# Kernel tuning notes

Measured on AMD Instinct MI355X. Metric: run time of the kernel, lower is better.

## Reference

```python
import jax, jax.numpy as jnp
import numpy as np

B, D_IN, H1, H2, A = 8192, 512, 4096, 4096, 64
QMIN, QMAX = -128.0, 127.0  # int8 saturation range


def _int_vals(key, shape, spread):
    # integer-valued fixed-point tensor stored as float32
    return jnp.clip(jnp.round(jax.random.normal(key, shape) * spread), QMIN * spread, QMAX * spread).astype(jnp.float32)


def setup_inputs() -> dict:
    key = jax.random.key(0)
    ks = jax.random.split(key, 9)
    x = jnp.clip(jnp.round(jax.random.normal(ks[0], (B, D_IN)) * 32.0), QMIN, QMAX).astype(jnp.float32)
    w1 = jnp.clip(jnp.round(jax.random.normal(ks[1], (H1, D_IN)) * 16.0), QMIN, QMAX).astype(jnp.float32)
    b1 = _int_vals(ks[2], (H1,), 256.0)
    w2 = jnp.clip(jnp.round(jax.random.normal(ks[3], (H2, H1)) * 16.0), QMIN, QMAX).astype(jnp.float32)
    b2 = _int_vals(ks[4], (H2,), 256.0)
    w_mu = jnp.clip(jnp.round(jax.random.normal(ks[5], (A, H2)) * 16.0), QMIN, QMAX).astype(jnp.float32)
    b_mu = _int_vals(ks[6], (A,), 256.0)
    w_prob = jnp.clip(jnp.round(jax.random.normal(ks[7], (A, H2)) * 16.0), QMIN, QMAX).astype(jnp.float32)
    b_prob = _int_vals(ks[8], (A,), 256.0)
    M = jnp.full((1,), 2.0 ** -10, dtype=jnp.float32)  # per-layer requant multiplier
    s = jnp.full((1,), 0.05, dtype=jnp.float32)        # activation quantize scale
    return {
        "x": x, "w1": w1, "b1": b1, "w2": w2, "b2": b2,
        "w_mu": w_mu, "b_mu": b_mu, "w_prob": w_prob, "b_prob": b_prob,
        "M1": M, "M2": M, "M_mu": M, "M_prob": M,
        "s2": s, "s_mu": s, "s_prob": s,
    }


def _qlinear(x, w, b, M):
    # genesys fixed-point linear: int accumulate then requantize by multiplier M
    acc = jnp.matmul(x, w.T) + b  # integer-valued fp32 accumulator
    return jnp.round(M * acc)


def _quantize(src, scale, zero_point=0.0):
    return jnp.clip(jnp.round(src / scale) + zero_point, QMIN, QMAX)


def reference(x, w1, b1, w2, b2, w_mu, b_mu, w_prob, b_prob, M1, M2, M_mu, M_prob, s2, s_mu, s_prob):
    h = jax.nn.relu(_qlinear(x, w1, b1, M1))
    h = _quantize(h, s2)
    h = jax.nn.relu(_qlinear(h, w2, b2, M2))
    # NOTE: original forward_int feeds the un-quantized relu output into the
    # heads (x_mu/x_prob quantizations are dead code) and returns only prob.
    prob = _qlinear(h, w_prob, b_prob, M_prob)
    return prob
```

## Files before the change

### kernel.cpp

```cpp
#include <hip/hip_runtime.h>
#include <stdint.h>

#define NB   8192
#define DIN  512
#define NH1  4096
#define NH2  4096
#define NA   64

typedef int v4i __attribute__((ext_vector_type(4)));

__device__ __forceinline__ v4i mfma_i8(v4i a, v4i b, v4i c) {
    return __builtin_amdgcn_mfma_i32_16x16x64_i8(a, b, c, 0, 0, 0);
}

__device__ __forceinline__ void gload16(const void* g, const void* l) {
    __builtin_amdgcn_global_load_lds(
        (const __attribute__((address_space(1))) void*)(uintptr_t)g,
        (__attribute__((address_space(3))) void*)(uint32_t)(uintptr_t)l,
        16, 0, 0);
}

__global__ void cvt_i8(const float* __restrict__ in, signed char* __restrict__ out, int n4) {
    const int i = blockIdx.x * blockDim.x + threadIdx.x;
    if (i >= n4) return;
    const float4 v = ((const float4*)in)[i];
    char4 c;
    c.x = (signed char)__float2int_rn(v.x);
    c.y = (signed char)__float2int_rn(v.y);
    c.z = (signed char)__float2int_rn(v.z);
    c.w = (signed char)__float2int_rn(v.w);
    ((char4*)out)[i] = c;
}

__global__ void sum_wp(const float* __restrict__ wp, int* __restrict__ S) {
    __shared__ int red[256];
    const int a = blockIdx.x, t = threadIdx.x;
    int p = 0;
    for (int k = t; k < NH2; k += 256) p += __float2int_rn(wp[(size_t)a * NH2 + k]);
    red[t] = p; __syncthreads();
    for (int s = 128; s > 0; s >>= 1) { if (t < s) red[t] += red[t + s]; __syncthreads(); }
    if (t == 0) S[a] = red[0];
}

template <int EPI>
__global__ __launch_bounds__(256, 2)
void gemm_pl(const signed char* __restrict__ Ag,
             const signed char* __restrict__ Bg,
             int M, int N, int K,
             const float* __restrict__ bias,
             const float* __restrict__ Mscale,
             const float* __restrict__ qscale,
             signed char* __restrict__ out0,
             signed char* __restrict__ out1)
{
    __shared__ __align__(16) signed char lds[3][24576];

    const int tid  = threadIdx.x;
    const int lane = tid & 63;
    const int wid  = tid >> 6;
    const int wm   = wid >> 1, wn = wid & 1;

    const int nwg  = gridDim.x;
    const int bid  = blockIdx.x;
    const int swzb = (bid & 7) * (nwg >> 3) + (bid >> 3);
    const int nbx  = N >> 7;
    const int bx   = swzb % nbx;
    const int by   = swzb / nbx;
    const int bm0  = by << 8, bn0 = bx << 7;

    const int srow = tid >> 2;
    const int sc   = (((tid & 3) ^ ((tid >> 3) & 3)) << 4);
    const signed char* aS = Ag + (size_t)(bm0 + srow) * K + sc;
    const signed char* bS = Bg + (size_t)(bn0 + srow) * K + sc;
    const size_t sK = (size_t)64 * K;

#define STG(bp, t) do { \
    const int ko_ = (t) << 6; \
    gload16(aS + ko_,          &lds[bp][0]     + tid * 16); \
    gload16(aS + sK + ko_,     &lds[bp][4096]  + tid * 16); \
    gload16(aS + 2 * sK + ko_, &lds[bp][8192]  + tid * 16); \
    gload16(aS + 3 * sK + ko_, &lds[bp][12288] + tid * 16); \
    gload16(bS + ko_,          &lds[bp][16384] + tid * 16); \
    gload16(bS + sK + ko_,     &lds[bp][20480] + tid * 16); } while (0)

    const int r    = lane & 15;
    const int pc   = (((lane >> 4) ^ ((r >> 1) & 3)) << 4);
    const int aoff = wm * 8192 + r * 64 + pc;
    const int boff = 16384 + wn * 4096 + r * 64 + pc;

    const int nt = K >> 6;

    STG(0, 0);
    STG(1, 1);
    asm volatile("s_waitcnt vmcnt(6)" ::: "memory");
    __builtin_amdgcn_s_barrier();

    v4i af[8], bf[4];
    {
        const signed char* L = &lds[0][0];
        #pragma unroll
        for (int m = 0; m < 8; ++m) af[m] = *(const v4i*)(L + aoff + m * 1024);
        #pragma unroll
        for (int n = 0; n < 4; ++n) bf[n] = *(const v4i*)(L + boff + n * 1024);
    }

    v4i acc[8][4] = {};
    int cur = 0;

    for (int t = 0; t < nt; ++t) {
        if (t + 2 < nt) {
            const int nb = (cur == 0) ? 2 : cur - 1;
            STG(nb, t + 2);
            asm volatile("s_waitcnt vmcnt(6)" ::: "memory");
        } else {
            asm volatile("s_waitcnt vmcnt(0)" ::: "memory");
        }
        __builtin_amdgcn_s_barrier();

        const int nxt = (cur == 2) ? 0 : cur + 1;
        const signed char* Ln = &lds[nxt][0];

        __builtin_amdgcn_s_setprio(1);
        #pragma unroll
        for (int m = 0; m < 8; ++m) {
            #pragma unroll
            for (int n = 0; n < 4; ++n)
                acc[m][n] = mfma_i8(af[m], bf[n], acc[m][n]);
            af[m] = *(const v4i*)(Ln + aoff + m * 1024);
        }
        __builtin_amdgcn_s_setprio(0);
        #pragma unroll
        for (int n = 0; n < 4; ++n) bf[n] = *(const v4i*)(Ln + boff + n * 1024);

        __builtin_amdgcn_s_barrier();
        cur = nxt;
    }
#undef STG

    __syncthreads();
    signed char* img0 = (signed char*)&lds[0][0];
    signed char* img1 = img0 + 36864;
    const int fr = (lane >> 4) << 2;
    const int fc = lane & 15;

#define FLUSH(dst, img) do { \
    _Pragma("unroll") \
    for (int p = 0; p < 8; ++p) { \
        const int idx = p * 256 + tid; \
        const int row = idx >> 3, ch = (idx & 7) << 4; \
        *(int4*)((dst) + (size_t)(bm0 + row) * N + bn0 + ch) = *(const int4*)((img) + row * 144 + ch); \
    } } while (0)

    if constexpr (EPI == 1) {
        const float Mv = Mscale[0];
        const float sv = qscale[0];
        #pragma unroll
        for (int n = 0; n < 4; ++n) {
            const int ecol = wn * 64 + n * 16 + fc;
            const int bint = __float2int_rn(bias[bn0 + ecol]);
            #pragma unroll
            for (int m = 0; m < 8; ++m) {
                const int erow = wm * 128 + m * 16 + fr;
                #pragma unroll
                for (int j = 0; j < 4; ++j) {
                    const int accv = acc[m][n][j] + bint;
                    float h = rintf(Mv * (float)accv);
                    h = fmaxf(h, 0.0f);
                    float q = rintf(h / sv);
                    q = fminf(fmaxf(q, -128.0f), 127.0f);
                    img0[(erow + j) * 144 + ecol] = (signed char)(int)q;
                }
            }
        }
        __syncthreads();
        FLUSH(out0, img0);
    } else {
        const float Mv = Mscale[0];
        #pragma unroll
        for (int n = 0; n < 4; ++n) {
            const int ecol = wn * 64 + n * 16 + fc;
            const int bint = __float2int_rn(bias[bn0 + ecol]);
            #pragma unroll
            for (int m = 0; m < 8; ++m) {
                const int erow = wm * 128 + m * 16 + fr;
                #pragma unroll
                for (int j = 0; j < 4; ++j) {
                    const int accv = acc[m][n][j] + bint;
                    double rr = rint((double)Mv * (double)accv);
                    rr = rr > 0.0 ? rr : 0.0;
                    const int v = (int)rr;
                    img0[(erow + j) * 144 + ecol] = (signed char)((v & 255) - 128);
                    img1[(erow + j) * 144 + ecol] = (signed char)((v >> 8) - 128);
                }
            }
        }
        __syncthreads();
        FLUSH(out0, img0);
        FLUSH(out1, img1);
    }
#undef FLUSH
}

__global__ __launch_bounds__(512, 1)
void head_mfma(const signed char* __restrict__ lo,
               const signed char* __restrict__ hi,
               const signed char* __restrict__ wpq,
               int* __restrict__ part)
{
    __shared__ __align__(16) signed char Bl[32768];
    __shared__ __align__(16) signed char Al[3][32768];

    const int tid  = threadIdx.x;
    const int lane = tid & 63;
    const int wid  = tid >> 6;
    const int rblk = blockIdx.x >> 3;
    const int kblk = blockIdx.x & 7;
    const int bm0  = rblk << 8;
    const int kb   = kblk << 9;

    #pragma unroll
    for (int s = 0; s < 4; ++s) {
        const int brow = s * 16 + (tid >> 5);
        const int pch  = tid & 31;
        const int lc   = pch ^ (brow & 7);
        gload16(wpq + (size_t)brow * NH2 + kb + lc * 16, Bl + brow * 512 + pch * 16);
    }

    const int srow  = tid >> 2;
    const int sclog = (tid & 3) ^ ((tid >> 3) & 3);
    const size_t ab = (size_t)(bm0 + srow) * NH2 + kb + sclog * 16;
    const size_t rK = (size_t)128 * NH2;

    #define HSTAGE(bp, ko) do { \
        gload16(lo + ab + (ko),      &Al[bp][0]     + tid * 16); \
        gload16(lo + ab + rK + (ko), &Al[bp][8192]  + tid * 16); \
        gload16(hi + ab + (ko),      &Al[bp][16384] + tid * 16); \
        gload16(hi + ab + rK + (ko), &Al[bp][24576] + tid * 16); } while (0)

    HSTAGE(0, 0);
    HSTAGE(1, 64);

    const int r    = lane & 15;
    const int cg   = lane >> 4;
    const int pcA  = (cg ^ ((r >> 1) & 3)) * 16;
    const int aoff = wid * 2048 + r * 64 + pcA;

    v4i accL[2][4] = {}, accH[2][4] = {};
    int cur = 0, nxt = 2;

    for (int t = 0; t < 8; ++t) {
        if (t < 7) asm volatile("s_waitcnt vmcnt(4)" ::: "memory");
        else       asm volatile("s_waitcnt vmcnt(0)" ::: "memory");
        __builtin_amdgcn_s_barrier();

        const signed char* A = &Al[cur][0];
        v4i bf[4], al[2], ah[2];
        #pragma unroll
        for (int n = 0; n < 4; ++n)
            bf[n] = *(const v4i*)(Bl + (n * 16 + r) * 512 + (((t * 4 + cg) ^ (r & 7)) * 16));
        #pragma unroll
        for (int m = 0; m < 2; ++m) al[m] = *(const v4i*)(A + aoff + m * 1024);
        #pragma unroll
        for (int m = 0; m < 2; ++m) ah[m] = *(const v4i*)(A + 16384 + aoff + m * 1024);

        if (t + 2 < 8) HSTAGE(nxt, (t + 2) << 6);

        __builtin_amdgcn_s_setprio(1);
        #pragma unroll
        for (int m = 0; m < 2; ++m)
            #pragma unroll
            for (int n = 0; n < 4; ++n) {
                accL[m][n] = mfma_i8(al[m], bf[n], accL[m][n]);
                accH[m][n] = mfma_i8(ah[m], bf[n], accH[m][n]);
            }
        __builtin_amdgcn_s_setprio(0);
        __builtin_amdgcn_s_barrier();

        cur = (cur == 2) ? 0 : cur + 1;
        nxt = (nxt == 2) ? 0 : nxt + 1;
    }
    #undef HSTAGE

    int* pb = part + (size_t)kblk * (NB * NA);
    const int rowb = bm0 + wid * 32 + ((lane >> 4) << 2);
    #pragma unroll
    for (int m = 0; m < 2; ++m)
        #pragma unroll
        for (int n = 0; n < 4; ++n) {
            const int a = n * 16 + (lane & 15);
            #pragma unroll
            for (int j = 0; j < 4; ++j) {
                const int row = rowb + m * 16 + j;
                pb[(size_t)row * NA + a] = accL[m][n][j] + (accH[m][n][j] << 8);
            }
        }
}

__global__ __launch_bounds__(256)
void comb_head(const int* __restrict__ part, const int* __restrict__ S,
               const float* __restrict__ bp, const float* __restrict__ Mp,
               float* __restrict__ out)
{
    const int t = blockIdx.x * 256 + threadIdx.x;
    const int a = t & 63;
    long long sum = 0;
    #pragma unroll
    for (int c = 0; c < 8; ++c) sum += part[(size_t)c * (NB * NA) + t];
    sum += 32896LL * (long long)S[a] + (long long)__float2int_rn(bp[a]);
    out[t] = (float)rint((double)Mp[0] * (double)sum);
}

extern "C" void kernel_launch(void* const* d_in, const int* in_sizes, int n_in,
                              void* d_out, int out_size, void* d_ws, size_t ws_size,
                              hipStream_t stream) {
    const float* x  = (const float*)d_in[0];
    const float* w1 = (const float*)d_in[1];
    const float* b1 = (const float*)d_in[2];
    const float* w2 = (const float*)d_in[3];
    const float* b2 = (const float*)d_in[4];
    const float* wp = (const float*)d_in[7];
    const float* bp = (const float*)d_in[8];
    const float* M1 = (const float*)d_in[9];
    const float* M2 = (const float*)d_in[10];
    const float* Mp = (const float*)d_in[12];
    const float* s2 = (const float*)d_in[13];

    const size_t MB = (size_t)1 << 20;
    char* ws = (char*)d_ws;
    signed char* x_i8  = (signed char*)(ws);
    signed char* w1_i8 = (signed char*)(ws + 4  * MB);
    signed char* w2_i8 = (signed char*)(ws + 6  * MB);
    signed char* wp_i8 = (signed char*)(ws + 22 * MB);
    int*         Ssum  = (int*)        (ws + 22 * MB + 512 * 1024);
    signed char* h1q   = (signed char*)(ws + 23 * MB);
    signed char* h2lo  = (signed char*)(ws + 55 * MB);
    signed char* h2hi  = (signed char*)(ws + 87 * MB);
    int*         part  = (int*)        (ws);

    cvt_i8<<<dim3(4096),  dim3(256), 0, stream>>>(x,  x_i8,  NB  * DIN / 4);
    cvt_i8<<<dim3(2048),  dim3(256), 0, stream>>>(w1, w1_i8, NH1 * DIN / 4);
    cvt_i8<<<dim3(16384), dim3(256), 0, stream>>>(w2, w2_i8, NH2 * NH1 / 4);
    cvt_i8<<<dim3(256),   dim3(256), 0, stream>>>(wp, wp_i8, NA  * NH2 / 4);
    sum_wp<<<dim3(64), dim3(256), 0, stream>>>(wp, Ssum);

    gemm_pl<1><<<dim3((NB / 256) * (NH1 / 128)), dim3(256), 0, stream>>>(
        x_i8, w1_i8, NB, NH1, DIN, b1, M1, s2, h1q, nullptr);
    gemm_pl<2><<<dim3((NB / 256) * (NH2 / 128)), dim3(256), 0, stream>>>(
        h1q, w2_i8, NB, NH2, NH1, b2, M2, nullptr, h2lo, h2hi);
    head_mfma<<<dim3(256), dim3(512), 0, stream>>>(h2lo, h2hi, wp_i8, part);
    comb_head<<<dim3(NB * NA / 256), dim3(256), 0, stream>>>(part, Ssum, bp, Mp, (float*)d_out);
}
```

Before: 223.2 us.

## Split GEMM block across eight waves with 64x64 per-wave tiles

The int8 MFMA GEMM keeps its 256x128 block tile but now runs 512 threads (8 waves) instead of 256. Each wave computes a 64x64 sub-tile instead of 128x64, which halves its accumulator and A-fragment registers, and each thread issues three staging loads per K step instead of six. The trailing barrier in the main loop is removed, relying on the triple buffer and the leading barrier for safety, and the epilogue image and flush are remapped to the new wave layout with 8-byte stores. This aims for more latency hiding and less synchronisation, at the cost of more LDS fragment reads per MFMA and narrower global stores.

```diff
diff --git a/kernel.cpp b/kernel.cpp
--- a/kernel.cpp
+++ b/kernel.cpp
@@ -43,8 +43,8 @@
 }
 
 template <int EPI>
-__global__ __launch_bounds__(256, 2)
-void gemm_pl(const signed char* __restrict__ Ag,
+__global__ __launch_bounds__(512, 4)
+void gemm_ra(const signed char* __restrict__ Ag,
              const signed char* __restrict__ Bg,
              int M, int N, int K,
              const float* __restrict__ bias,
@@ -72,46 +72,43 @@
     const int sc   = (((tid & 3) ^ ((tid >> 3) & 3)) << 4);
     const signed char* aS = Ag + (size_t)(bm0 + srow) * K + sc;
     const signed char* bS = Bg + (size_t)(bn0 + srow) * K + sc;
-    const size_t sK = (size_t)64 * K;
+    const size_t rK = (size_t)128 * K;
 
 #define STG(bp, t) do { \
     const int ko_ = (t) << 6; \
-    gload16(aS + ko_,          &lds[bp][0]     + tid * 16); \
-    gload16(aS + sK + ko_,     &lds[bp][4096]  + tid * 16); \
-    gload16(aS + 2 * sK + ko_, &lds[bp][8192]  + tid * 16); \
-    gload16(aS + 3 * sK + ko_, &lds[bp][12288] + tid * 16); \
-    gload16(bS + ko_,          &lds[bp][16384] + tid * 16); \
-    gload16(bS + sK + ko_,     &lds[bp][20480] + tid * 16); } while (0)
+    gload16(aS + ko_,      &lds[bp][0]     + tid * 16); \
+    gload16(aS + rK + ko_, &lds[bp][8192]  + tid * 16); \
+    gload16(bS + ko_,      &lds[bp][16384] + tid * 16); } while (0)
 
     const int r    = lane & 15;
     const int pc   = (((lane >> 4) ^ ((r >> 1) & 3)) << 4);
-    const int aoff = wm * 8192 + r * 64 + pc;
+    const int aoff = wm * 4096 + r * 64 + pc;
     const int boff = 16384 + wn * 4096 + r * 64 + pc;
 
     const int nt = K >> 6;
 
     STG(0, 0);
     STG(1, 1);
-    asm volatile("s_waitcnt vmcnt(6)" ::: "memory");
+    asm volatile("s_waitcnt vmcnt(3)" ::: "memory");
     __builtin_amdgcn_s_barrier();
 
-    v4i af[8], bf[4];
+    v4i af[4], bf[4];
     {
         const signed char* L = &lds[0][0];
         #pragma unroll
-        for (int m = 0; m < 8; ++m) af[m] = *(const v4i*)(L + aoff + m * 1024);
+        for (int m = 0; m < 4; ++m) af[m] = *(const v4i*)(L + aoff + m * 1024);
         #pragma unroll
         for (int n = 0; n < 4; ++n) bf[n] = *(const v4i*)(L + boff + n * 1024);
     }
 
-    v4i acc[8][4] = {};
+    v4i acc[4][4] = {};
     int cur = 0;
 
     for (int t = 0; t < nt; ++t) {
         if (t + 2 < nt) {
             const int nb = (cur == 0) ? 2 : cur - 1;
             STG(nb, t + 2);
-            asm volatile("s_waitcnt vmcnt(6)" ::: "memory");
+            asm volatile("s_waitcnt vmcnt(3)" ::: "memory");
         } else {
             asm volatile("s_waitcnt vmcnt(0)" ::: "memory");
         }
@@ -122,7 +119,7 @@
 
         __builtin_amdgcn_s_setprio(1);
         #pragma unroll
-        for (int m = 0; m < 8; ++m) {
+        for (int m = 0; m < 4; ++m) {
             #pragma unroll
             for (int n = 0; n < 4; ++n)
                 acc[m][n] = mfma_i8(af[m], bf[n], acc[m][n]);
@@ -132,23 +129,24 @@
         #pragma unroll
         for (int n = 0; n < 4; ++n) bf[n] = *(const v4i*)(Ln + boff + n * 1024);
 
-        __builtin_amdgcn_s_barrier();
         cur = nxt;
     }
 #undef STG
 
     __syncthreads();
     signed char* img0 = (signed char*)&lds[0][0];
-    signed char* img1 = img0 + 36864;
-    const int fr = (lane >> 4) << 2;
-    const int fc = lane & 15;
+    signed char* img1 = img0 + 34816;
+    const int rowb = wm * 64 + ((lane >> 4) << 2);
+    const int colb = wn * 64 + (lane & 15);
 
 #define FLUSH(dst, img) do { \
     _Pragma("unroll") \
     for (int p = 0; p < 8; ++p) { \
-        const int idx = p * 256 + tid; \
-        const int row = idx >> 3, ch = (idx & 7) << 4; \
-        *(int4*)((dst) + (size_t)(bm0 + row) * N + bn0 + ch) = *(const int4*)((img) + row * 144 + ch); \
+        const int idx = p * 512 + tid; \
+        const int row = idx >> 4; \
+        const int cb  = (idx & 15) * 8; \
+        *(int2*)((dst) + (size_t)(bm0 + row) * N + bn0 + cb) = \
+            *(const int2*)((img) + row * 136 + cb); \
     } } while (0)
 
     if constexpr (EPI == 1) {
@@ -156,19 +154,19 @@
         const float sv = qscale[0];
         #pragma unroll
         for (int n = 0; n < 4; ++n) {
-            const int ecol = wn * 64 + n * 16 + fc;
-            const int bint = __float2int_rn(bias[bn0 + ecol]);
-            #pragma unroll
-            for (int m = 0; m < 8; ++m) {
-                const int erow = wm * 128 + m * 16 + fr;
+            const int col  = colb + n * 16;
+            const int bint = __float2int_rn(bias[bn0 + col]);
+            #pragma unroll
+            for (int m = 0; m < 4; ++m) {
                 #pragma unroll
                 for (int j = 0; j < 4; ++j) {
+                    const int row  = rowb + m * 16 + j;
                     const int accv = acc[m][n][j] + bint;
                     float h = rintf(Mv * (float)accv);
                     h = fmaxf(h, 0.0f);
                     float q = rintf(h / sv);
                     q = fminf(fmaxf(q, -128.0f), 127.0f);
-                    img0[(erow + j) * 144 + ecol] = (signed char)(int)q;
+                    img0[row * 136 + col] = (signed char)(int)q;
                 }
             }
         }
@@ -178,19 +176,19 @@
         const float Mv = Mscale[0];
         #pragma unroll
         for (int n = 0; n < 4; ++n) {
-            const int ecol = wn * 64 + n * 16 + fc;
-            const int bint = __float2int_rn(bias[bn0 + ecol]);
-            #pragma unroll
-            for (int m = 0; m < 8; ++m) {
-                const int erow = wm * 128 + m * 16 + fr;
+            const int col  = colb + n * 16;
+            const int bint = __float2int_rn(bias[bn0 + col]);
+            #pragma unroll
+            for (int m = 0; m < 4; ++m) {
                 #pragma unroll
                 for (int j = 0; j < 4; ++j) {
+                    const int row  = rowb + m * 16 + j;
                     const int accv = acc[m][n][j] + bint;
                     double rr = rint((double)Mv * (double)accv);
                     rr = rr > 0.0 ? rr : 0.0;
                     const int v = (int)rr;
-                    img0[(erow + j) * 144 + ecol] = (signed char)((v & 255) - 128);
-                    img1[(erow + j) * 144 + ecol] = (signed char)((v >> 8) - 128);
+                    img0[row * 136 + col] = (signed char)((v & 255) - 128);
+                    img1[row * 136 + col] = (signed char)((v >> 8) - 128);
                 }
             }
         }
@@ -343,9 +341,9 @@
     cvt_i8<<<dim3(256),   dim3(256), 0, stream>>>(wp, wp_i8, NA  * NH2 / 4);
     sum_wp<<<dim3(64), dim3(256), 0, stream>>>(wp, Ssum);
 
-    gemm_pl<1><<<dim3((NB / 256) * (NH1 / 128)), dim3(256), 0, stream>>>(
+    gemm_ra<1><<<dim3((NB / 256) * (NH1 / 128)), dim3(512), 0, stream>>>(
         x_i8, w1_i8, NB, NH1, DIN, b1, M1, s2, h1q, nullptr);
-    gemm_pl<2><<<dim3((NB / 256) * (NH2 / 128)), dim3(256), 0, stream>>>(
+    gemm_ra<2><<<dim3((NB / 256) * (NH2 / 128)), dim3(512), 0, stream>>>(
         h1q, w2_i8, NB, NH2, NH1, b2, M2, nullptr, h2lo, h2hi);
     head_mfma<<<dim3(256), dim3(512), 0, stream>>>(h2lo, h2hi, wp_i8, part);
     comb_head<<<dim3(NB * NA / 256), dim3(256), 0, stream>>>(part, Ssum, bp, Mp, (float*)d_out);
```

New measurement: 230.1 us. 3.1% more time.
